# Optimization experiments

Measured on AMD Instinct MI355X. Metric: run time of the kernel, lower is better.

## Reference

```python
import jax, jax.numpy as jnp
import numpy as np

C_IN = 256
C_BN = 64


def conv1x1(x, w, b):
    # x: [B, Cin, H, W], w: [Cout, Cin], b: [Cout] -> [B, Cout, H, W]
    return jnp.einsum('oc,bchw->bohw', w, x) + b[None, :, None, None]


def setup_inputs() -> dict:
    key = jax.random.key(0)
    ks = jax.random.split(key, 9)
    B, H, W = 4, 64, 64
    s_in = 1.0 / np.sqrt(C_IN)
    s_bn = 1.0 / np.sqrt(C_BN)
    return {
        'x': jax.random.normal(ks[0], (B, C_IN, H, W), jnp.float32),
        'w_k': jax.random.uniform(ks[1], (C_BN, C_IN), jnp.float32, -s_in, s_in),
        'b_k': jax.random.uniform(ks[2], (C_BN,), jnp.float32, -s_in, s_in),
        'w_q': jax.random.uniform(ks[3], (C_BN, C_IN), jnp.float32, -s_in, s_in),
        'b_q': jax.random.uniform(ks[4], (C_BN,), jnp.float32, -s_in, s_in),
        'w_v': jax.random.uniform(ks[5], (C_BN, C_IN), jnp.float32, -s_in, s_in),
        'b_v': jax.random.uniform(ks[6], (C_BN,), jnp.float32, -s_in, s_in),
        'w_u': jax.random.uniform(ks[7], (C_IN, C_BN), jnp.float32, -s_bn, s_bn),
        'b_u': jax.random.uniform(ks[8], (C_IN,), jnp.float32, -s_bn, s_bn),
    }


def reference(x, w_k, b_k, w_q, b_q, w_v, b_v, w_u, b_u):
    B, C, H, W = x.shape
    N = H * W
    xk = conv1x1(x, w_k, b_k).reshape(B, C_BN, N)            # [B, d, N]
    xq = conv1x1(x, w_q, b_q).reshape(B, C_BN, N)            # [B, d, N]
    xv = conv1x1(x, w_v, b_v).reshape(B, C_BN, N)            # [B, d, N]
    qk = jnp.einsum('bdi,bdk->bik', xq, xk)                  # [B, N, N]
    attn = jax.nn.softmax(qk, axis=2)                        # softmax over keys
    out = jnp.einsum('bik,bdk->bdi', attn, xv)               # [B, d, N]
    out = out.reshape(B, C_BN, H, W)
    y = conv1x1(out, w_u, b_u)                               # [B, C, H, W]
    return x + y
```

## Files before the change

### kernel.cpp

```cpp
#include <hip/hip_runtime.h>
#include <math.h>

#define N_TOK 4096
#define CIN 256
#define CBN 64
#define LOG2E 1.44269504f

typedef __attribute__((ext_vector_type(8))) short bf16x8;
typedef __attribute__((ext_vector_type(4))) float f32x4;

static __device__ __forceinline__ unsigned short f2bf(float f) {
    union { float f; unsigned u; } v; v.f = f;
    unsigned r = v.u + 0x7fffu + ((v.u >> 16) & 1u);
    return (unsigned short)(r >> 16);
}
static __device__ __forceinline__ unsigned pack2(float a, float b) {
    return (unsigned)f2bf(a) | ((unsigned)f2bf(b) << 16);
}

__global__ __launch_bounds__(256) void prep_w(
        const float* __restrict__ wq, const float* __restrict__ wk,
        const float* __restrict__ wv, const float* __restrict__ wu,
        const float* __restrict__ bq,
        short* __restrict__ Wb, short* __restrict__ Wu, float* __restrict__ bqs) {
    int idx = blockIdx.x * 256 + threadIdx.x;
    int d = idx >> 8, c = idx & 255;
    Wb[d * 256 + c]         = (short)f2bf(wq[idx] * LOG2E);
    Wb[(64 + d) * 256 + c]  = (short)f2bf(wk[idx]);
    Wb[(128 + d) * 256 + c] = (short)f2bf(wv[idx]);
    Wu[idx] = (short)f2bf(wu[idx]);
    if (idx < 64) bqs[idx] = bq[idx] * LOG2E;
}

__global__ __launch_bounds__(256) void qkv_kernel(
        const float* __restrict__ x, const short* __restrict__ Wb,
        const float* __restrict__ bqs, const float* __restrict__ bk, const float* __restrict__ bv,
        short* __restrict__ Qt, short* __restrict__ Kt, short* __restrict__ Vd) {
    int t = threadIdx.x;
    int blk = blockIdx.x;
    int b = blk >> 8;
    int n0 = (blk & 255) * 16;

    __shared__ short Xs[16][264];

    {
        int tok4 = t & 3;
        int cb = t >> 2;
        const float* xb = x + (size_t)b * CIN * N_TOK + n0 + tok4 * 4;
        #pragma unroll
        for (int p = 0; p < 4; ++p) {
            int c = p * 64 + cb;
            float4 xv = *(const float4*)(xb + (size_t)c * N_TOK);
            float xs[4] = {xv.x, xv.y, xv.z, xv.w};
            #pragma unroll
            for (int i = 0; i < 4; ++i)
                Xs[tok4 * 4 + i][c] = (short)f2bf(xs[i]);
        }
    }
    __syncthreads();

    int w = t >> 6;
    int g = (t >> 4) & 3;
    int lr = t & 15;

    f32x4 acc[3];
    #pragma unroll
    for (int m = 0; m < 3; ++m) acc[m] = (f32x4){0.f, 0.f, 0.f, 0.f};
    const short* wbase = Wb + (size_t)(w * 16 + lr) * 256 + 8 * g;
    #pragma unroll
    for (int ks = 0; ks < 8; ++ks) {
        bf16x8 xf = *(const bf16x8*)&Xs[lr][ks * 32 + 8 * g];
        #pragma unroll
        for (int m = 0; m < 3; ++m) {
            bf16x8 wf = *(const bf16x8*)(wbase + (size_t)m * 64 * 256 + ks * 32);
            acc[m] = __builtin_amdgcn_mfma_f32_16x16x32_bf16(wf, xf, acc[m], 0, 0, 0);
        }
    }
    int d0 = w * 16 + 4 * g;
    int tok = n0 + lr;
    float4 bq4 = *(const float4*)(bqs + d0);
    float4 bk4 = *(const float4*)(bk + d0);
    float4 bv4 = *(const float4*)(bv + d0);
    size_t qo = ((size_t)b * N_TOK + tok) * 64 + d0;
    uint2 qp, kp;
    qp.x = pack2(acc[0][0] + bq4.x, acc[0][1] + bq4.y);
    qp.y = pack2(acc[0][2] + bq4.z, acc[0][3] + bq4.w);
    kp.x = pack2(acc[1][0] + bk4.x, acc[1][1] + bk4.y);
    kp.y = pack2(acc[1][2] + bk4.z, acc[1][3] + bk4.w);
    *(uint2*)(Qt + qo) = qp;
    *(uint2*)(Kt + qo) = kp;
    int u = tok & 31;
    int vcol = (tok & ~31) + 8 * ((u >> 2) & 3) + 4 * (u >> 4) + (u & 3);
    float bvr[4] = {bv4.x, bv4.y, bv4.z, bv4.w};
    #pragma unroll
    for (int r = 0; r < 4; ++r)
        Vd[((size_t)b * 64 + d0 + r) * N_TOK + vcol] = (short)f2bf(acc[2][r] + bvr[r]);
}

__global__ __launch_bounds__(1024, 4) void attn_kernel(
        const short* __restrict__ Qt, const short* __restrict__ Kt,
        const short* __restrict__ Vsw, short* __restrict__ Otm) {
    int t = threadIdx.x;
    int w = t >> 6;
    int qt_l = w >> 2;
    int sp = w & 3;
    int g = (t >> 4) & 3;
    int lr = t & 15;
    int l = t & 63;

    int bid = blockIdx.x;
    int blk = ((bid & 7) << 5) | (bid >> 3);
    int qtg = blk * 4 + qt_l;
    int b = qtg >> 8;
    int q0 = (qtg & 255) * 16;

    const short* Qb = Qt + (size_t)b * N_TOK * 64;
    const short* Kb = Kt + (size_t)b * N_TOK * 64;
    const short* Vb = Vsw + (size_t)b * 64 * N_TOK;

    __shared__ __align__(16) char LB[4][2][16384];
    __shared__ float Ml[16][16];

    bf16x8 qf0 = *(const bf16x8*)(Qb + (q0 + lr) * 64 + 8 * g);
    bf16x8 qf1 = *(const bf16x8*)(Qb + (q0 + lr) * 64 + 32 + 8 * g);

    f32x4 o[4];
    #pragma unroll
    for (int mt = 0; mt < 4; ++mt) o[mt] = (f32x4){0.f, 0.f, 0.f, 0.f};
    float lacc = 0.f;

    int rr = l >> 3;
    int cx8 = ((l & 7) ^ rr) * 8;

    auto STAGE = [&](int kt, int buf) {
        int k0 = sp * 1024 + kt * 64;
        char* dst0 = &LB[sp][buf][0];
        #pragma unroll
        for (int j = 0; j < 4; ++j) {
            int seg = qt_l * 4 + j;
            const short* src;
            if (seg < 8)
                src = Kb + (size_t)(k0 + seg * 8 + rr) * 64 + cx8;
            else
                src = Vb + (size_t)((seg - 8) * 8 + rr) * N_TOK + k0 + cx8;
            __builtin_amdgcn_global_load_lds(
                (const __attribute__((address_space(1))) void*)src,
                (__attribute__((address_space(3))) void*)(dst0 + seg * 1024),
                16, 0, 0);
        }
    };

    STAGE(0, 0);
    __syncthreads();

    int xk = lr & 7;
    int cA = (g ^ xk) << 4;
    int cur = 0;
    for (int kt = 0; kt < 16; ++kt) {
        if (kt < 15) STAGE(kt + 1, cur ^ 1);
        const char* KB_ = &LB[sp][cur][0];
        const char* VB_ = KB_ + 8192;
        f32x4 s[4];
        #pragma unroll
        for (int nt = 0; nt < 4; ++nt) {
            const char* rp = KB_ + (nt * 16 + lr) * 128;
            bf16x8 kf0 = *(const bf16x8*)(rp + cA);
            bf16x8 kf1 = *(const bf16x8*)(rp + (cA ^ 64));
            f32x4 z = (f32x4){0.f, 0.f, 0.f, 0.f};
            z = __builtin_amdgcn_mfma_f32_16x16x32_bf16(kf0, qf0, z, 0, 0, 0);
            s[nt] = __builtin_amdgcn_mfma_f32_16x16x32_bf16(kf1, qf1, z, 0, 0, 0);
        }
        #pragma unroll
        for (int nt = 0; nt < 4; ++nt)
            #pragma unroll
            for (int r = 0; r < 4; ++r) {
                float p = __builtin_amdgcn_exp2f(s[nt][r]);
                s[nt][r] = p;
                lacc += p;
            }
        bf16x8 bp0, bp1;
        #pragma unroll
        for (int e = 0; e < 8; ++e) {
            bp0[e] = (short)f2bf(s[e >> 2][e & 3]);
            bp1[e] = (short)f2bf(s[2 + (e >> 2)][e & 3]);
        }
        #pragma unroll
        for (int mt = 0; mt < 4; ++mt) {
            const char* rp = VB_ + (mt * 16 + lr) * 128;
            bf16x8 av0 = *(const bf16x8*)(rp + cA);
            bf16x8 av1 = *(const bf16x8*)(rp + (cA ^ 64));
            o[mt] = __builtin_amdgcn_mfma_f32_16x16x32_bf16(av0, bp0, o[mt], 0, 0, 0);
            o[mt] = __builtin_amdgcn_mfma_f32_16x16x32_bf16(av1, bp1, o[mt], 0, 0, 0);
        }
        __syncthreads();
        cur ^= 1;
    }
    lacc += __shfl_xor(lacc, 16);
    lacc += __shfl_xor(lacc, 32);
    float* OmL = (float*)&LB[0][0][0];
    #pragma unroll
    for (int mt = 0; mt < 4; ++mt)
        *(f32x4*)(OmL + (w * 16 + lr) * 64 + mt * 16 + 4 * g) = o[mt];
    Ml[w][lr] = lacc;
    __syncthreads();
    {
        int qt2 = t >> 8, q = (t >> 4) & 15, dq = t & 15;
        float a0 = 0.f, a1 = 0.f, a2 = 0.f, a3 = 0.f, lsum = 0.f;
        #pragma unroll
        for (int s2 = 0; s2 < 4; ++s2) {
            const float* pp = OmL + ((qt2 * 4 + s2) * 16 + q) * 64 + dq * 4;
            float4 v = *(const float4*)pp;
            a0 += v.x; a1 += v.y; a2 += v.z; a3 += v.w;
            lsum += Ml[qt2 * 4 + s2][q];
        }
        float inv = 1.f / lsum;
        int qtg2 = blk * 4 + qt2;
        int b2 = qtg2 >> 8;
        int tok = (qtg2 & 255) * 16 + q;
        uint2 ow;
        ow.x = pack2(a0 * inv, a1 * inv);
        ow.y = pack2(a2 * inv, a3 * inv);
        *(uint2*)(Otm + ((size_t)b2 * N_TOK + tok) * 64 + dq * 4) = ow;
    }
}

__global__ __launch_bounds__(256) void out_kernel(
        const short* __restrict__ Otm, const short* __restrict__ Wu,
        const float* __restrict__ bu, const float* __restrict__ x,
        float* __restrict__ y) {
    int t = threadIdx.x;
    int w = t >> 6, g = (t >> 4) & 3, lr = t & 15;
    int blk = blockIdx.x;
    int b = blk >> 8;
    int rem = blk & 255;
    int nblk = rem >> 2, cblk = rem & 3;
    int n0 = nblk * 64 + w * 16;
    int c0 = cblk * 64;

    const short* Ob = Otm + ((size_t)b * N_TOK + n0) * 64;
    bf16x8 a0 = *(const bf16x8*)(Ob + lr * 64 + 8 * g);
    bf16x8 a1 = *(const bf16x8*)(Ob + lr * 64 + 32 + 8 * g);

    #pragma unroll
    for (int ct = 0; ct < 4; ++ct) {
        int c = c0 + ct * 16 + lr;
        const short* wp = Wu + (size_t)c * 64 + 8 * g;
        bf16x8 b0 = *(const bf16x8*)wp;
        bf16x8 b1 = *(const bf16x8*)(wp + 32);
        f32x4 acc = (f32x4){0.f, 0.f, 0.f, 0.f};
        acc = __builtin_amdgcn_mfma_f32_16x16x32_bf16(a0, b0, acc, 0, 0, 0);
        acc = __builtin_amdgcn_mfma_f32_16x16x32_bf16(a1, b1, acc, 0, 0, 0);
        float bc = bu[c];
        size_t base = ((size_t)b * CIN + c) * N_TOK + n0 + 4 * g;
        float4 xr = *(const float4*)(x + base);
        float4 yo;
        yo.x = acc[0] + bc + xr.x;
        yo.y = acc[1] + bc + xr.y;
        yo.z = acc[2] + bc + xr.z;
        yo.w = acc[3] + bc + xr.w;
        *(float4*)(y + base) = yo;
    }
}

extern "C" void kernel_launch(void* const* d_in, const int* in_sizes, int n_in,
                              void* d_out, int out_size, void* d_ws, size_t ws_size,
                              hipStream_t stream) {
    const float* x  = (const float*)d_in[0];
    const float* wk = (const float*)d_in[1];
    const float* bk = (const float*)d_in[2];
    const float* wq = (const float*)d_in[3];
    const float* bq = (const float*)d_in[4];
    const float* wv = (const float*)d_in[5];
    const float* bv = (const float*)d_in[6];
    const float* wu = (const float*)d_in[7];
    const float* bu = (const float*)d_in[8];
    float* out = (float*)d_out;

    char* ws = (char*)d_ws;
    if (ws_size < (size_t)(9u << 20)) return;
    short* Qt  = (short*)(ws);
    short* Kt  = (short*)(ws + (2u << 20));
    short* Vd  = (short*)(ws + (4u << 20));
    short* Otm = (short*)(ws + (6u << 20));
    short* Wb  = (short*)(ws + (8u << 20));
    short* Wu  = Wb + 192 * 256;
    float* bqs = (float*)(Wu + 256 * 64);

    prep_w<<<dim3(64), dim3(256), 0, stream>>>(wq, wk, wv, wu, bq, Wb, Wu, bqs);
    qkv_kernel<<<dim3(1024), dim3(256), 0, stream>>>(x, Wb, bqs, bk, bv, Qt, Kt, Vd);
    attn_kernel<<<dim3(256), dim3(1024), 0, stream>>>(Qt, Kt, Vd, Otm);
    out_kernel<<<dim3(1024), dim3(256), 0, stream>>>(Otm, Wu, bu, x, out);
}
```

Baseline: 66.05 us.

## Reuse K/V tiles across two query tiles per wave and double QKV token tile

The attention kernel now assigns each wave two 16-query tiles and splits keys across 8 waves instead of 4, so each staged K/V fragment feeds twice as many MFMAs and LDS traffic per FLOP drops. The K/V staging is reorganised into 32-key chunks with separate K and V loaders and a new V swizzle. The QKV projection kernel processes 32 tokens per block, reusing each weight fragment for two MFMAs and halving the grid. In exchange, register pressure rises and the cross-wave reduction over 8 splits grows.

Result: faster. 61.79 us (-6.4%).

```diff
diff --git a/kernel.cpp b/kernel.cpp
--- a/kernel.cpp
+++ b/kernel.cpp
@@ -38,18 +38,18 @@
         short* __restrict__ Qt, short* __restrict__ Kt, short* __restrict__ Vd) {
     int t = threadIdx.x;
     int blk = blockIdx.x;
-    int b = blk >> 8;
-    int n0 = (blk & 255) * 16;
-
-    __shared__ short Xs[16][264];
+    int b = blk >> 7;
+    int n0 = (blk & 127) * 32;
+
+    __shared__ short Xs[32][264];
 
     {
-        int tok4 = t & 3;
-        int cb = t >> 2;
+        int tok4 = t & 7;
+        int cb = t >> 3;
         const float* xb = x + (size_t)b * CIN * N_TOK + n0 + tok4 * 4;
         #pragma unroll
-        for (int p = 0; p < 4; ++p) {
-            int c = p * 64 + cb;
+        for (int p = 0; p < 8; ++p) {
+            int c = p * 32 + cb;
             float4 xv = *(const float4*)(xb + (size_t)c * N_TOK);
             float xs[4] = {xv.x, xv.y, xv.z, xv.w};
             #pragma unroll
@@ -63,38 +63,45 @@
     int g = (t >> 4) & 3;
     int lr = t & 15;
 
-    f32x4 acc[3];
-    #pragma unroll
-    for (int m = 0; m < 3; ++m) acc[m] = (f32x4){0.f, 0.f, 0.f, 0.f};
+    f32x4 acc[3][2];
+    #pragma unroll
+    for (int m = 0; m < 3; ++m)
+        #pragma unroll
+        for (int st = 0; st < 2; ++st) acc[m][st] = (f32x4){0.f, 0.f, 0.f, 0.f};
     const short* wbase = Wb + (size_t)(w * 16 + lr) * 256 + 8 * g;
     #pragma unroll
     for (int ks = 0; ks < 8; ++ks) {
-        bf16x8 xf = *(const bf16x8*)&Xs[lr][ks * 32 + 8 * g];
+        bf16x8 xf0 = *(const bf16x8*)&Xs[lr][ks * 32 + 8 * g];
+        bf16x8 xf1 = *(const bf16x8*)&Xs[16 + lr][ks * 32 + 8 * g];
         #pragma unroll
         for (int m = 0; m < 3; ++m) {
             bf16x8 wf = *(const bf16x8*)(wbase + (size_t)m * 64 * 256 + ks * 32);
-            acc[m] = __builtin_amdgcn_mfma_f32_16x16x32_bf16(wf, xf, acc[m], 0, 0, 0);
+            acc[m][0] = __builtin_amdgcn_mfma_f32_16x16x32_bf16(wf, xf0, acc[m][0], 0, 0, 0);
+            acc[m][1] = __builtin_amdgcn_mfma_f32_16x16x32_bf16(wf, xf1, acc[m][1], 0, 0, 0);
         }
     }
     int d0 = w * 16 + 4 * g;
-    int tok = n0 + lr;
     float4 bq4 = *(const float4*)(bqs + d0);
     float4 bk4 = *(const float4*)(bk + d0);
     float4 bv4 = *(const float4*)(bv + d0);
-    size_t qo = ((size_t)b * N_TOK + tok) * 64 + d0;
-    uint2 qp, kp;
-    qp.x = pack2(acc[0][0] + bq4.x, acc[0][1] + bq4.y);
-    qp.y = pack2(acc[0][2] + bq4.z, acc[0][3] + bq4.w);
-    kp.x = pack2(acc[1][0] + bk4.x, acc[1][1] + bk4.y);
-    kp.y = pack2(acc[1][2] + bk4.z, acc[1][3] + bk4.w);
-    *(uint2*)(Qt + qo) = qp;
-    *(uint2*)(Kt + qo) = kp;
-    int u = tok & 31;
-    int vcol = (tok & ~31) + 8 * ((u >> 2) & 3) + 4 * (u >> 4) + (u & 3);
     float bvr[4] = {bv4.x, bv4.y, bv4.z, bv4.w};
     #pragma unroll
-    for (int r = 0; r < 4; ++r)
-        Vd[((size_t)b * 64 + d0 + r) * N_TOK + vcol] = (short)f2bf(acc[2][r] + bvr[r]);
+    for (int st = 0; st < 2; ++st) {
+        int tok = n0 + st * 16 + lr;
+        size_t qo = ((size_t)b * N_TOK + tok) * 64 + d0;
+        uint2 qp, kp;
+        qp.x = pack2(acc[0][st][0] + bq4.x, acc[0][st][1] + bq4.y);
+        qp.y = pack2(acc[0][st][2] + bq4.z, acc[0][st][3] + bq4.w);
+        kp.x = pack2(acc[1][st][0] + bk4.x, acc[1][st][1] + bk4.y);
+        kp.y = pack2(acc[1][st][2] + bk4.z, acc[1][st][3] + bk4.w);
+        *(uint2*)(Qt + qo) = qp;
+        *(uint2*)(Kt + qo) = kp;
+        int u = tok & 31;
+        int vcol = (tok & ~31) + 8 * ((u >> 2) & 3) + 4 * (u >> 4) + (u & 3);
+        #pragma unroll
+        for (int r = 0; r < 4; ++r)
+            Vd[((size_t)b * 64 + d0 + r) * N_TOK + vcol] = (short)f2bf(acc[2][st][r] + bvr[r]);
+    }
 }
 
 __global__ __launch_bounds__(1024, 4) void attn_kernel(
@@ -102,125 +109,143 @@
         const short* __restrict__ Vsw, short* __restrict__ Otm) {
     int t = threadIdx.x;
     int w = t >> 6;
-    int qt_l = w >> 2;
-    int sp = w & 3;
+    int wq = w >> 3;
+    int sp = w & 7;
     int g = (t >> 4) & 3;
     int lr = t & 15;
     int l = t & 63;
 
     int bid = blockIdx.x;
     int blk = ((bid & 7) << 5) | (bid >> 3);
-    int qtg = blk * 4 + qt_l;
-    int b = qtg >> 8;
-    int q0 = (qtg & 255) * 16;
+    int b = blk >> 6;
+    int q0 = (blk & 63) * 64;
 
     const short* Qb = Qt + (size_t)b * N_TOK * 64;
     const short* Kb = Kt + (size_t)b * N_TOK * 64;
     const short* Vb = Vsw + (size_t)b * 64 * N_TOK;
 
-    __shared__ __align__(16) char LB[4][2][16384];
-    __shared__ float Ml[16][16];
-
-    bf16x8 qf0 = *(const bf16x8*)(Qb + (q0 + lr) * 64 + 8 * g);
-    bf16x8 qf1 = *(const bf16x8*)(Qb + (q0 + lr) * 64 + 32 + 8 * g);
-
-    f32x4 o[4];
-    #pragma unroll
-    for (int mt = 0; mt < 4; ++mt) o[mt] = (f32x4){0.f, 0.f, 0.f, 0.f};
-    float lacc = 0.f;
-
-    int rr = l >> 3;
-    int cx8 = ((l & 7) ^ rr) * 8;
+    __shared__ __align__(16) char LB[8][2][8192];
+    __shared__ float Ml[32][16];
+
+    bf16x8 qf[2][2];
+    #pragma unroll
+    for (int j = 0; j < 2; ++j) {
+        const short* qp = Qb + (q0 + (wq * 2 + j) * 16 + lr) * 64 + 8 * g;
+        qf[j][0] = *(const bf16x8*)qp;
+        qf[j][1] = *(const bf16x8*)(qp + 32);
+    }
+
+    f32x4 o[2][4];
+    #pragma unroll
+    for (int j = 0; j < 2; ++j)
+        #pragma unroll
+        for (int mt = 0; mt < 4; ++mt) o[j][mt] = (f32x4){0.f, 0.f, 0.f, 0.f};
+    float la0 = 0.f, la1 = 0.f;
+
+    int krow = l >> 3;
+    int kchk = ((l & 7) ^ krow) * 8;
+    int vrow = l >> 2;
+    int vchk = ((l & 3) ^ (vrow & 3)) * 8;
 
     auto STAGE = [&](int kt, int buf) {
-        int k0 = sp * 1024 + kt * 64;
+        int k0s = sp * 512 + kt * 32;
         char* dst0 = &LB[sp][buf][0];
-        #pragma unroll
-        for (int j = 0; j < 4; ++j) {
-            int seg = qt_l * 4 + j;
-            const short* src;
-            if (seg < 8)
-                src = Kb + (size_t)(k0 + seg * 8 + rr) * 64 + cx8;
-            else
-                src = Vb + (size_t)((seg - 8) * 8 + rr) * N_TOK + k0 + cx8;
-            __builtin_amdgcn_global_load_lds(
-                (const __attribute__((address_space(1))) void*)src,
-                (__attribute__((address_space(3))) void*)(dst0 + seg * 1024),
-                16, 0, 0);
+        if (wq == 0) {
+            #pragma unroll
+            for (int j = 0; j < 4; ++j) {
+                const short* src = Kb + (size_t)(k0s + j * 8 + krow) * 64 + kchk;
+                __builtin_amdgcn_global_load_lds(
+                    (const __attribute__((address_space(1))) void*)src,
+                    (__attribute__((address_space(3))) void*)(dst0 + j * 1024),
+                    16, 0, 0);
+            }
+        } else {
+            #pragma unroll
+            for (int j = 0; j < 4; ++j) {
+                const short* src = Vb + (size_t)(j * 16 + vrow) * N_TOK + k0s + vchk;
+                __builtin_amdgcn_global_load_lds(
+                    (const __attribute__((address_space(1))) void*)src,
+                    (__attribute__((address_space(3))) void*)(dst0 + 4096 + j * 1024),
+                    16, 0, 0);
+            }
         }
     };
 
     STAGE(0, 0);
     __syncthreads();
 
-    int xk = lr & 7;
-    int cA = (g ^ xk) << 4;
+    int cK = (g ^ (lr & 7)) << 4;
+    int cV = (g ^ (lr & 3)) << 4;
     int cur = 0;
     for (int kt = 0; kt < 16; ++kt) {
         if (kt < 15) STAGE(kt + 1, cur ^ 1);
         const char* KB_ = &LB[sp][cur][0];
-        const char* VB_ = KB_ + 8192;
-        f32x4 s[4];
-        #pragma unroll
-        for (int nt = 0; nt < 4; ++nt) {
+        const char* VB_ = KB_ + 4096;
+        f32x4 s[2][2];
+        #pragma unroll
+        for (int nt = 0; nt < 2; ++nt) {
             const char* rp = KB_ + (nt * 16 + lr) * 128;
-            bf16x8 kf0 = *(const bf16x8*)(rp + cA);
-            bf16x8 kf1 = *(const bf16x8*)(rp + (cA ^ 64));
-            f32x4 z = (f32x4){0.f, 0.f, 0.f, 0.f};
-            z = __builtin_amdgcn_mfma_f32_16x16x32_bf16(kf0, qf0, z, 0, 0, 0);
-            s[nt] = __builtin_amdgcn_mfma_f32_16x16x32_bf16(kf1, qf1, z, 0, 0, 0);
-        }
-        #pragma unroll
-        for (int nt = 0; nt < 4; ++nt)
+            bf16x8 kf0 = *(const bf16x8*)(rp + cK);
+            bf16x8 kf1 = *(const bf16x8*)(rp + (cK ^ 64));
+            #pragma unroll
+            for (int j = 0; j < 2; ++j) {
+                f32x4 z = (f32x4){0.f, 0.f, 0.f, 0.f};
+                z = __builtin_amdgcn_mfma_f32_16x16x32_bf16(kf0, qf[j][0], z, 0, 0, 0);
+                s[j][nt] = __builtin_amdgcn_mfma_f32_16x16x32_bf16(kf1, qf[j][1], z, 0, 0, 0);
+            }
+        }
+        #pragma unroll
+        for (int nt = 0; nt < 2; ++nt)
             #pragma unroll
             for (int r = 0; r < 4; ++r) {
-                float p = __builtin_amdgcn_exp2f(s[nt][r]);
-                s[nt][r] = p;
-                lacc += p;
+                float p0 = __builtin_amdgcn_exp2f(s[0][nt][r]);
+                float p1 = __builtin_amdgcn_exp2f(s[1][nt][r]);
+                s[0][nt][r] = p0; la0 += p0;
+                s[1][nt][r] = p1; la1 += p1;
             }
-        bf16x8 bp0, bp1;
+        bf16x8 bp[2];
         #pragma unroll
         for (int e = 0; e < 8; ++e) {
-            bp0[e] = (short)f2bf(s[e >> 2][e & 3]);
-            bp1[e] = (short)f2bf(s[2 + (e >> 2)][e & 3]);
+            bp[0][e] = (short)f2bf(s[0][e >> 2][e & 3]);
+            bp[1][e] = (short)f2bf(s[1][e >> 2][e & 3]);
         }
         #pragma unroll
         for (int mt = 0; mt < 4; ++mt) {
-            const char* rp = VB_ + (mt * 16 + lr) * 128;
-            bf16x8 av0 = *(const bf16x8*)(rp + cA);
-            bf16x8 av1 = *(const bf16x8*)(rp + (cA ^ 64));
-            o[mt] = __builtin_amdgcn_mfma_f32_16x16x32_bf16(av0, bp0, o[mt], 0, 0, 0);
-            o[mt] = __builtin_amdgcn_mfma_f32_16x16x32_bf16(av1, bp1, o[mt], 0, 0, 0);
+            bf16x8 av = *(const bf16x8*)(VB_ + (mt * 16 + lr) * 64 + cV);
+            o[0][mt] = __builtin_amdgcn_mfma_f32_16x16x32_bf16(av, bp[0], o[0][mt], 0, 0, 0);
+            o[1][mt] = __builtin_amdgcn_mfma_f32_16x16x32_bf16(av, bp[1], o[1][mt], 0, 0, 0);
         }
         __syncthreads();
         cur ^= 1;
     }
-    lacc += __shfl_xor(lacc, 16);
-    lacc += __shfl_xor(lacc, 32);
+    la0 += __shfl_xor(la0, 16); la0 += __shfl_xor(la0, 32);
+    la1 += __shfl_xor(la1, 16); la1 += __shfl_xor(la1, 32);
     float* OmL = (float*)&LB[0][0][0];
     #pragma unroll
-    for (int mt = 0; mt < 4; ++mt)
-        *(f32x4*)(OmL + (w * 16 + lr) * 64 + mt * 16 + 4 * g) = o[mt];
-    Ml[w][lr] = lacc;
+    for (int j = 0; j < 2; ++j) {
+        int qt = wq * 2 + j;
+        #pragma unroll
+        for (int mt = 0; mt < 4; ++mt)
+            *(f32x4*)(OmL + ((qt * 8 + sp) * 16 + lr) * 64 + mt * 16 + 4 * g) = o[j][mt];
+        Ml[qt * 8 + sp][lr] = j == 0 ? la0 : la1;
+    }
     __syncthreads();
     {
         int qt2 = t >> 8, q = (t >> 4) & 15, dq = t & 15;
         float a0 = 0.f, a1 = 0.f, a2 = 0.f, a3 = 0.f, lsum = 0.f;
         #pragma unroll
-        for (int s2 = 0; s2 < 4; ++s2) {
-            const float* pp = OmL + ((qt2 * 4 + s2) * 16 + q) * 64 + dq * 4;
+        for (int s2 = 0; s2 < 8; ++s2) {
+            const float* pp = OmL + ((qt2 * 8 + s2) * 16 + q) * 64 + dq * 4;
             float4 v = *(const float4*)pp;
             a0 += v.x; a1 += v.y; a2 += v.z; a3 += v.w;
-            lsum += Ml[qt2 * 4 + s2][q];
+            lsum += Ml[qt2 * 8 + s2][q];
         }
         float inv = 1.f / lsum;
-        int qtg2 = blk * 4 + qt2;
-        int b2 = qtg2 >> 8;
-        int tok = (qtg2 & 255) * 16 + q;
+        int tok = q0 + qt2 * 16 + q;
         uint2 ow;
         ow.x = pack2(a0 * inv, a1 * inv);
         ow.y = pack2(a2 * inv, a3 * inv);
-        *(uint2*)(Otm + ((size_t)b2 * N_TOK + tok) * 64 + dq * 4) = ow;
+        *(uint2*)(Otm + ((size_t)b * N_TOK + tok) * 64 + dq * 4) = ow;
     }
 }
 
@@ -287,7 +312,7 @@
     float* bqs = (float*)(Wu + 256 * 64);
 
     prep_w<<<dim3(64), dim3(256), 0, stream>>>(wq, wk, wv, wu, bq, Wb, Wu, bqs);
-    qkv_kernel<<<dim3(1024), dim3(256), 0, stream>>>(x, Wb, bqs, bk, bv, Qt, Kt, Vd);
+    qkv_kernel<<<dim3(512), dim3(256), 0, stream>>>(x, Wb, bqs, bk, bv, Qt, Kt, Vd);
     attn_kernel<<<dim3(256), dim3(1024), 0, stream>>>(Qt, Kt, Vd, Otm);
     out_kernel<<<dim3(1024), dim3(256), 0, stream>>>(Otm, Wu, bu, x, out);
 }
```
